# Performance work log

Hardware: AMD Instinct MI355X
Metric: run time of the kernel (lower is better)

Reference implementation:

```python
import jax, jax.numpy as jnp
import numpy as np

HEADS = 4
DIM_HEAD = 32
SCALE = 10.0
EPS = 1e-12  # F.normalize eps


def setup_inputs() -> dict:
    key = jax.random.key(0)
    k0, k1, k2 = jax.random.split(key, 3)
    b, c, h, w = 4, 256, 64, 64
    hidden = HEADS * DIM_HEAD  # 128
    x = jax.random.normal(k0, (b, c, h, w), dtype=jnp.float32)
    # 1x1 convs == per-pixel linear layers; store as [out_ch, in_ch]
    w_qkv = jax.random.normal(k1, (3 * hidden, c), dtype=jnp.float32) * (1.0 / np.sqrt(c))
    w_out = jax.random.normal(k2, (c, hidden), dtype=jnp.float32) * (1.0 / np.sqrt(hidden))
    b_out = jnp.zeros((c,), dtype=jnp.float32)
    return {"x": x, "w_qkv": w_qkv, "w_out": w_out, "b_out": b_out}


def _l2norm(t):
    # normalize along the per-head feature dim d (axis=2 of [b,h,d,n])
    n = jnp.sqrt(jnp.sum(t * t, axis=2, keepdims=True))
    return t / jnp.maximum(n, EPS)


def reference(x, w_qkv, w_out, b_out):
    b, c, h, w = x.shape
    n = h * w
    # to_qkv 1x1 conv (no bias)
    qkv = jnp.einsum('oc,bchw->bohw', w_qkv, x)          # [b, 3*hidden, h, w]
    qkv = qkv.reshape(b, 3, HEADS, DIM_HEAD, n)          # chunk dim=1 then split heads
    q, k, v = qkv[:, 0], qkv[:, 1], qkv[:, 2]            # each [b, heads, d, n]
    q = _l2norm(q)
    k = _l2norm(k)
    sim = jnp.einsum('bhdi,bhdj->bhij', q, k) * SCALE    # [b, heads, n, n]
    attn = jax.nn.softmax(sim, axis=-1)
    out = jnp.einsum('bhij,bhdj->bhid', attn, v)         # [b, heads, n, d]
    # 'b h (x y) d -> b (h d) x y'
    out = out.transpose(0, 1, 3, 2).reshape(b, HEADS * DIM_HEAD, h, w)
    # to_out 1x1 conv with bias
    return jnp.einsum('oc,bchw->bohw', w_out, out) + b_out[None, :, None, None]
```

## Files before the change

### kernel.cpp

```cpp
#include <hip/hip_runtime.h>
#include <math.h>

#define BB 4
#define CC 256
#define NHEAD 4
#define DH 32
#define NN 4096
#define HID 128

typedef _Float16 f16;
typedef _Float16 f16x8 __attribute__((ext_vector_type(8)));
typedef _Float16 f16x4 __attribute__((ext_vector_type(4)));
typedef float f32x4 __attribute__((ext_vector_type(4)));

#define QPRESCALE 14.42695041f
#define NSHIFT 14.42695041f

#if __has_builtin(__builtin_amdgcn_exp2f)
#define EXP2F(x) __builtin_amdgcn_exp2f(x)
#else
#define EXP2F(x) __expf((x)*0.6931471805599453f)
#endif

__device__ __forceinline__ f16x8 cvt8(const float* p) {
    float4 a = *(const float4*)p;
    float4 b = *(const float4*)(p + 4);
    f16x8 r;
    r[0] = (f16)a.x; r[1] = (f16)a.y; r[2] = (f16)a.z; r[3] = (f16)a.w;
    r[4] = (f16)b.x; r[5] = (f16)b.y; r[6] = (f16)b.z; r[7] = (f16)b.w;
    return r;
}

__global__ __launch_bounds__(256) void qkv_fused(const float* __restrict__ x,
                                                 const float* __restrict__ wq,
                                                 f16* __restrict__ qh,
                                                 f16* __restrict__ kh,
                                                 f16* __restrict__ vh) {
    int wave = threadIdx.x >> 6, lane = threadIdx.x & 63;
    int quad = lane >> 4, col = lane & 15;
    int b = blockIdx.z;
    int o0 = blockIdx.y * 64;
    int i0 = blockIdx.x * 128 + wave * 32;
    const float* xb = x + (size_t)b * CC * NN;

    f32x4 c[4][2];
#pragma unroll
    for (int mt = 0; mt < 4; mt++)
#pragma unroll
        for (int nt = 0; nt < 2; nt++) c[mt][nt] = f32x4{0.f, 0.f, 0.f, 0.f};

#pragma unroll
    for (int k0 = 0; k0 < CC; k0 += 32) {
        f16x8 a[4];
#pragma unroll
        for (int mt = 0; mt < 4; mt++)
            a[mt] = cvt8(wq + (size_t)(o0 + mt * 16 + col) * CC + k0 + quad * 8);
#pragma unroll
        for (int nt = 0; nt < 2; nt++) {
            const float* xc = xb + (size_t)(k0 + quad * 8) * NN + i0 + nt * 16 + col;
            f16x8 bf;
#pragma unroll
            for (int j = 0; j < 8; j++) bf[j] = (f16)xc[(size_t)j * NN];
#pragma unroll
            for (int mt = 0; mt < 4; mt++)
                c[mt][nt] = __builtin_amdgcn_mfma_f32_16x16x32_f16(a[mt], bf, c[mt][nt], 0, 0, 0);
        }
    }

    if (o0 < 256) {
        int isQ = (o0 < 128);
        int obase = isQ ? o0 : (o0 - 128);
        f16* dst = isQ ? qh : kh;
        float pre = isQ ? QPRESCALE : 1.0f;
#pragma unroll
        for (int nt = 0; nt < 2; nt++) {
#pragma unroll
            for (int hh = 0; hh < 2; hh++) {
                float ss = 0.f;
#pragma unroll
                for (int m2 = 0; m2 < 2; m2++)
#pragma unroll
                    for (int r = 0; r < 4; r++) {
                        float v = c[hh * 2 + m2][nt][r];
                        ss = fmaf(v, v, ss);
                    }
                ss += __shfl_xor(ss, 16);
                ss += __shfl_xor(ss, 32);
                float inv = pre / fmaxf(sqrtf(ss), 1e-12f);
                int h = (obase + hh * 32) >> 5;
                size_t row = ((size_t)(b * 4 + h) * NN + i0 + nt * 16 + col) * 32;
#pragma unroll
                for (int m2 = 0; m2 < 2; m2++) {
                    f16x4 st;
#pragma unroll
                    for (int r = 0; r < 4; r++) st[r] = (f16)(c[hh * 2 + m2][nt][r] * inv);
                    *(f16x4*)(dst + row + m2 * 16 + quad * 4) = st;
                }
            }
        }
    } else {
        int o2 = o0 - 256;
#pragma unroll
        for (int nt = 0; nt < 2; nt++) {
            int i = i0 + nt * 16 + col;
#pragma unroll
            for (int mt = 0; mt < 4; mt++) {
                int h = (o2 + mt * 16) >> 5;
                int d = (mt & 1) * 16 + quad * 4;
#pragma unroll
                for (int r = 0; r < 4; r++)
                    vh[((size_t)(b * 4 + h) * 32 + d + r) * NN + i] = (f16)c[mt][nt][r];
            }
        }
    }
}

#define KROW 40
#define VROW 72

struct KV32 {
    f16x8 k0, k1;
    f16x4 v0n0, v0n1, v1n0, v1n1;
};

__device__ __forceinline__ KV32 lds_frags(const f16* kl, const f16* vl,
                                          int jb, int col, int quad) {
    KV32 f;
    f.k0 = *(const f16x8*)(kl + (jb + col) * KROW + quad * 8);
    f.k1 = *(const f16x8*)(kl + (jb + 16 + col) * KROW + quad * 8);
    f.v0n0 = *(const f16x4*)(vl + col * VROW + jb + quad * 4);
    f.v0n1 = *(const f16x4*)(vl + (16 + col) * VROW + jb + quad * 4);
    f.v1n0 = *(const f16x4*)(vl + col * VROW + jb + 16 + quad * 4);
    f.v1n1 = *(const f16x4*)(vl + (16 + col) * VROW + jb + 16 + quad * 4);
    return f;
}

__device__ __forceinline__ f16x4 expblk(f32x4 s, float& lacc) {
    float p0 = EXP2F(s[0]), p1 = EXP2F(s[1]);
    float p2 = EXP2F(s[2]), p3 = EXP2F(s[3]);
    lacc += (p0 + p1) + (p2 + p3);
    f16x4 r;
    r[0] = (f16)p0; r[1] = (f16)p1; r[2] = (f16)p2; r[3] = (f16)p3;
    return r;
}

__device__ __forceinline__ void compute32(const KV32& f, f16x8 qB0, f16x8 qB1,
                                          f32x4& o00, f32x4& o01,
                                          f32x4& o10, f32x4& o11,
                                          float& l0, float& l1) {
    const f32x4 zs = {-NSHIFT, -NSHIFT, -NSHIFT, -NSHIFT};
    f32x4 s00 = __builtin_amdgcn_mfma_f32_16x16x32_f16(f.k0, qB0, zs, 0, 0, 0);
    f32x4 s10 = __builtin_amdgcn_mfma_f32_16x16x32_f16(f.k0, qB1, zs, 0, 0, 0);
    f32x4 s01 = __builtin_amdgcn_mfma_f32_16x16x32_f16(f.k1, qB0, zs, 0, 0, 0);
    f32x4 s11 = __builtin_amdgcn_mfma_f32_16x16x32_f16(f.k1, qB1, zs, 0, 0, 0);
    f16x4 p00 = expblk(s00, l0);
    f16x4 p10 = expblk(s10, l1);
    f16x4 p01 = expblk(s01, l0);
    f16x4 p11 = expblk(s11, l1);
    o00 = __builtin_amdgcn_mfma_f32_16x16x16f16(p00, f.v0n0, o00, 0, 0, 0);
    o01 = __builtin_amdgcn_mfma_f32_16x16x16f16(p00, f.v0n1, o01, 0, 0, 0);
    o10 = __builtin_amdgcn_mfma_f32_16x16x16f16(p10, f.v0n0, o10, 0, 0, 0);
    o11 = __builtin_amdgcn_mfma_f32_16x16x16f16(p10, f.v0n1, o11, 0, 0, 0);
    o00 = __builtin_amdgcn_mfma_f32_16x16x16f16(p01, f.v1n0, o00, 0, 0, 0);
    o01 = __builtin_amdgcn_mfma_f32_16x16x16f16(p01, f.v1n1, o01, 0, 0, 0);
    o10 = __builtin_amdgcn_mfma_f32_16x16x16f16(p11, f.v1n0, o10, 0, 0, 0);
    o11 = __builtin_amdgcn_mfma_f32_16x16x16f16(p11, f.v1n1, o11, 0, 0, 0);
}

template <int SPLIT>
__global__ __launch_bounds__(256, 4) void attn_mfma(const f16* __restrict__ qh,
                                                    const f16* __restrict__ kh,
                                                    const f16* __restrict__ vh,
                                                    float* __restrict__ op,
                                                    float* __restrict__ lp,
                                                    f16* __restrict__ att16) {
    __shared__ __align__(16) f16 klds[2][64 * KROW];
    __shared__ __align__(16) f16 vlds[2][32 * VROW];
    int t = threadIdx.x;
    int wave = t >> 6, lane = t & 63;
    int quad = lane >> 4, col = lane & 15;

    int bid = blockIdx.x;
    int xcd = bid & 7;
    int slot = bid >> 3;
    int bh = xcd * 2 + slot / (32 * SPLIT);
    int rem = slot % (32 * SPLIT);
    int s = rem >> 5;
    int i0 = (rem & 31) * 128;
    int iw = i0 + wave * 32;

    const int NT = 64 / SPLIT;
    int kbase = s * (NN / SPLIT);

    const f16* qb = qh + (size_t)bh * NN * 32;
    const f16* kb = kh + (size_t)bh * NN * 32 + (size_t)kbase * 32;
    const f16* vb = vh + (size_t)bh * 32 * NN + kbase;

    f16x8 qB0 = *(const f16x8*)(qb + (size_t)(iw + col) * 32 + quad * 8);
    f16x8 qB1 = *(const f16x8*)(qb + (size_t)(iw + 16 + col) * 32 + quad * 8);

    f32x4 o00 = {0.f, 0.f, 0.f, 0.f}, o01 = o00, o10 = o00, o11 = o00;
    float l0 = 0.f, l1 = 0.f;

    int ktr = t >> 2, kts = t & 3;
    int vtr = t >> 3, vts = t & 7;

    f16x8 kr, vr;
    kr = *(const f16x8*)(kb + (size_t)(0 + ktr) * 32 + kts * 8);
    vr = *(const f16x8*)(vb + (size_t)vtr * NN + 0 + vts * 8);
    *(f16x8*)(&klds[0][0] + ktr * KROW + kts * 8) = kr;
    *(f16x8*)(&vlds[0][0] + vtr * VROW + vts * 8) = vr;
    __syncthreads();
    kr = *(const f16x8*)(kb + (size_t)(64 + ktr) * 32 + kts * 8);
    vr = *(const f16x8*)(vb + (size_t)vtr * NN + 64 + vts * 8);

    for (int tile = 0; tile < NT - 2; tile++) {
        int buf = tile & 1;
        const f16* kl = &klds[buf][0];
        const f16* vl = &vlds[buf][0];
        KV32 f0 = lds_frags(kl, vl, 0, col, quad);
        KV32 f1 = lds_frags(kl, vl, 32, col, quad);
        compute32(f0, qB0, qB1, o00, o01, o10, o11, l0, l1);
        compute32(f1, qB0, qB1, o00, o01, o10, o11, l0, l1);
        *(f16x8*)(&klds[buf ^ 1][0] + ktr * KROW + kts * 8) = kr;
        *(f16x8*)(&vlds[buf ^ 1][0] + vtr * VROW + vts * 8) = vr;
        __syncthreads();
        int j0 = (tile + 2) * 64;
        kr = *(const f16x8*)(kb + (size_t)(j0 + ktr) * 32 + kts * 8);
        vr = *(const f16x8*)(vb + (size_t)vtr * NN + j0 + vts * 8);
    }
    {
        KV32 f0 = lds_frags(&klds[0][0], &vlds[0][0], 0, col, quad);
        KV32 f1 = lds_frags(&klds[0][0], &vlds[0][0], 32, col, quad);
        compute32(f0, qB0, qB1, o00, o01, o10, o11, l0, l1);
        compute32(f1, qB0, qB1, o00, o01, o10, o11, l0, l1);
        *(f16x8*)(&klds[1][0] + ktr * KROW + kts * 8) = kr;
        *(f16x8*)(&vlds[1][0] + vtr * VROW + vts * 8) = vr;
        __syncthreads();
    }
    {
        KV32 f0 = lds_frags(&klds[1][0], &vlds[1][0], 0, col, quad);
        KV32 f1 = lds_frags(&klds[1][0], &vlds[1][0], 32, col, quad);
        compute32(f0, qB0, qB1, o00, o01, o10, o11, l0, l1);
        compute32(f1, qB0, qB1, o00, o01, o10, o11, l0, l1);
    }

    l0 += __shfl_xor(l0, 16); l0 += __shfl_xor(l0, 32);
    l1 += __shfl_xor(l1, 16); l1 += __shfl_xor(l1, 32);

    if constexpr (SPLIT == 1) {
        int b = bh >> 2, h = bh & 3;
        f16* ab = att16 + (size_t)b * NN * HID + h * 32;
#pragma unroll
        for (int r = 0; r < 4; r++) {
            float inv0 = __builtin_amdgcn_rcpf(__shfl(l0, quad * 4 + r));
            float inv1 = __builtin_amdgcn_rcpf(__shfl(l1, quad * 4 + r));
            size_t row0 = (size_t)(iw + quad * 4 + r) * HID;
            size_t row1 = (size_t)(iw + 16 + quad * 4 + r) * HID;
            ab[row0 + col]      = (f16)(o00[r] * inv0);
            ab[row0 + 16 + col] = (f16)(o01[r] * inv0);
            ab[row1 + col]      = (f16)(o10[r] * inv1);
            ab[row1 + 16 + col] = (f16)(o11[r] * inv1);
        }
    } else {
        float* ob = op + (size_t)(s * 16 + bh) * NN * 32;
#pragma unroll
        for (int r = 0; r < 4; r++) {
            size_t r0 = (size_t)(iw + quad * 4 + r) * 32;
            size_t r1 = (size_t)(iw + 16 + quad * 4 + r) * 32;
            ob[r0 + col]      = o00[r];
            ob[r0 + 16 + col] = o01[r];
            ob[r1 + col]      = o10[r];
            ob[r1 + 16 + col] = o11[r];
        }
        if (quad == 0) {
            lp[(size_t)(s * 16 + bh) * NN + iw + col]      = l0;
            lp[(size_t)(s * 16 + bh) * NN + iw + 16 + col] = l1;
        }
    }
}

__global__ __launch_bounds__(256) void attn_combine(const float* __restrict__ op,
                                                    const float* __restrict__ lp,
                                                    f16* __restrict__ att16,
                                                    int nsplit) {
    int gid = blockIdx.x * 256 + threadIdx.x;
    int rowid = gid >> 3;
    int seg = gid & 7;
    int bh = rowid >> 12;
    int q = rowid & 4095;

    float l = 0.f;
    f32x4 acc = {0.f, 0.f, 0.f, 0.f};
    for (int s = 0; s < nsplit; s++) {
        l += lp[(size_t)(s * 16 + bh) * NN + q];
        f32x4 a = *(const f32x4*)(op + ((size_t)(s * 16 + bh) * NN + q) * 32 + seg * 4);
        acc += a;
    }
    float inv = __builtin_amdgcn_rcpf(l);
    int b = bh >> 2, h = bh & 3;
    f16x4 st;
    st[0] = (f16)(acc[0] * inv);
    st[1] = (f16)(acc[1] * inv);
    st[2] = (f16)(acc[2] * inv);
    st[3] = (f16)(acc[3] * inv);
    *(f16x4*)(att16 + ((size_t)b * NN + q) * HID + h * 32 + seg * 4) = st;
}

__global__ __launch_bounds__(256) void out_mfma(const f16* __restrict__ att16,
                                                const float* __restrict__ wo,
                                                const float* __restrict__ bo,
                                                float* __restrict__ out) {
    int wave = threadIdx.x >> 6, lane = threadIdx.x & 63;
    int quad = lane >> 4, col = lane & 15;
    int b = blockIdx.z;
    int i0 = (blockIdx.x * 4 + wave) * 32;
    int o0 = blockIdx.y * 64;
    const f16* ab = att16 + (size_t)b * NN * HID;

    const f32x4 z = {0.f, 0.f, 0.f, 0.f};
    f32x4 c[2][4];
#pragma unroll
    for (int it = 0; it < 2; it++)
#pragma unroll
        for (int ot = 0; ot < 4; ot++) c[it][ot] = z;

#pragma unroll
    for (int k0 = 0; k0 < HID; k0 += 32) {
        f16x8 a0 = *(const f16x8*)(ab + (size_t)(i0 + col) * HID + k0 + quad * 8);
        f16x8 a1 = *(const f16x8*)(ab + (size_t)(i0 + 16 + col) * HID + k0 + quad * 8);
#pragma unroll
        for (int ot = 0; ot < 4; ot++) {
            f16x8 bf = cvt8(wo + (size_t)(o0 + ot * 16 + col) * HID + k0 + quad * 8);
            c[0][ot] = __builtin_amdgcn_mfma_f32_16x16x32_f16(a0, bf, c[0][ot], 0, 0, 0);
            c[1][ot] = __builtin_amdgcn_mfma_f32_16x16x32_f16(a1, bf, c[1][ot], 0, 0, 0);
        }
    }

#pragma unroll
    for (int it = 0; it < 2; it++)
#pragma unroll
        for (int ot = 0; ot < 4; ot++) {
            int o = o0 + ot * 16 + col;
            float bias = bo[o];
            int i = i0 + it * 16 + quad * 4;
            float4 st = {c[it][ot][0] + bias, c[it][ot][1] + bias,
                         c[it][ot][2] + bias, c[it][ot][3] + bias};
            *(float4*)(out + ((size_t)b * CC + o) * NN + i) = st;
        }
}

extern "C" void kernel_launch(void* const* d_in, const int* in_sizes, int n_in,
                              void* d_out, int out_size, void* d_ws, size_t ws_size,
                              hipStream_t stream) {
    const float* x     = (const float*)d_in[0];
    const float* w_qkv = (const float*)d_in[1];
    const float* w_out = (const float*)d_in[2];
    const float* b_out = (const float*)d_in[3];
    float* out = (float*)d_out;

    char* ws = (char*)d_ws;
    f16* qh    = (f16*)(ws);
    f16* kh    = (f16*)(ws + (4u << 20));
    f16* vh    = (f16*)(ws + (8u << 20));
    f16* att16 = (f16*)(ws + (12u << 20));

    qkv_fused<<<dim3(NN / 128, 384 / 64, BB), 256, 0, stream>>>(x, w_qkv, qh, kh, vh);

    if (ws_size >= (50ull << 20)) {
        float* op = (float*)(ws + (16ull << 20));
        float* lp = (float*)(ws + (48ull << 20));
        attn_mfma<4><<<dim3(2048), 256, 0, stream>>>(qh, kh, vh, op, lp, att16);
        attn_combine<<<dim3(2048), 256, 0, stream>>>(op, lp, att16, 4);
    } else if (ws_size >= (33ull << 20)) {
        float* op = (float*)(ws + (16ull << 20));
        float* lp = (float*)(ws + (32ull << 20));
        attn_mfma<2><<<dim3(1024), 256, 0, stream>>>(qh, kh, vh, op, lp, att16);
        attn_combine<<<dim3(2048), 256, 0, stream>>>(op, lp, att16, 2);
    } else {
        attn_mfma<1><<<dim3(512), 256, 0, stream>>>(qh, kh, vh, nullptr, nullptr, att16);
    }

    out_mfma<<<dim3(NN / 128, CC / 64, BB), 256, 0, stream>>>(att16, w_out, b_out, out);
}
```

Before: 165.3 us.

## Use K=32 MFMA for PV with permuted K rows and MFMA row-sum

```diff
diff --git a/kernel.cpp b/kernel.cpp
--- a/kernel.cpp
+++ b/kernel.cpp
@@ -11,7 +11,9 @@
 typedef _Float16 f16;
 typedef _Float16 f16x8 __attribute__((ext_vector_type(8)));
 typedef _Float16 f16x4 __attribute__((ext_vector_type(4)));
+typedef _Float16 f16x2 __attribute__((ext_vector_type(2)));
 typedef float f32x4 __attribute__((ext_vector_type(4)));
+typedef unsigned int u32x4 __attribute__((ext_vector_type(4)));
 
 #define QPRESCALE 14.42695041f
 #define NSHIFT 14.42695041f
@@ -118,53 +120,53 @@
 #define KROW 40
 #define VROW 72
 
-struct KV32 {
-    f16x8 k0, k1;
-    f16x4 v0n0, v0n1, v1n0, v1n1;
+struct G32 {
+    f16x8 kA, kB;
+    f16x8 v0, v1;
 };
 
-__device__ __forceinline__ KV32 lds_frags(const f16* kl, const f16* vl,
-                                          int jb, int col, int quad) {
-    KV32 f;
-    f.k0 = *(const f16x8*)(kl + (jb + col) * KROW + quad * 8);
-    f.k1 = *(const f16x8*)(kl + (jb + 16 + col) * KROW + quad * 8);
-    f.v0n0 = *(const f16x4*)(vl + col * VROW + jb + quad * 4);
-    f.v0n1 = *(const f16x4*)(vl + (16 + col) * VROW + jb + quad * 4);
-    f.v1n0 = *(const f16x4*)(vl + col * VROW + jb + 16 + quad * 4);
-    f.v1n1 = *(const f16x4*)(vl + (16 + col) * VROW + jb + 16 + quad * 4);
+__device__ __forceinline__ G32 lds_frags32(const f16* kl, const f16* vl,
+                                           int jb, int col, int quad) {
+    G32 f;
+    f.kA = *(const f16x8*)(kl + (jb + col) * KROW + quad * 8);
+    f.kB = *(const f16x8*)(kl + (jb + 16 + col) * KROW + quad * 8);
+    f.v0 = *(const f16x8*)(vl + col * VROW + jb + quad * 8);
+    f.v1 = *(const f16x8*)(vl + (16 + col) * VROW + jb + quad * 8);
     return f;
 }
 
-__device__ __forceinline__ f16x4 expblk(f32x4 s, float& lacc) {
-    float p0 = EXP2F(s[0]), p1 = EXP2F(s[1]);
-    float p2 = EXP2F(s[2]), p3 = EXP2F(s[3]);
-    lacc += (p0 + p1) + (p2 + p3);
-    f16x4 r;
-    r[0] = (f16)p0; r[1] = (f16)p1; r[2] = (f16)p2; r[3] = (f16)p3;
-    return r;
-}
-
-__device__ __forceinline__ void compute32(const KV32& f, f16x8 qB0, f16x8 qB1,
-                                          f32x4& o00, f32x4& o01,
-                                          f32x4& o10, f32x4& o11,
-                                          float& l0, float& l1) {
+__device__ __forceinline__ f16x8 expblk2(f32x4 sa, f32x4 sb) {
+    u32x4 w;
+    w[0] = __builtin_bit_cast(unsigned int,
+            __builtin_amdgcn_cvt_pkrtz(EXP2F(sa[0]), EXP2F(sa[1])));
+    w[1] = __builtin_bit_cast(unsigned int,
+            __builtin_amdgcn_cvt_pkrtz(EXP2F(sa[2]), EXP2F(sa[3])));
+    w[2] = __builtin_bit_cast(unsigned int,
+            __builtin_amdgcn_cvt_pkrtz(EXP2F(sb[0]), EXP2F(sb[1])));
+    w[3] = __builtin_bit_cast(unsigned int,
+            __builtin_amdgcn_cvt_pkrtz(EXP2F(sb[2]), EXP2F(sb[3])));
+    return __builtin_bit_cast(f16x8, w);
+}
+
+__device__ __forceinline__ void compute32g(const G32& f, f16x8 qB0, f16x8 qB1,
+                                           f32x4& o00, f32x4& o01,
+                                           f32x4& o10, f32x4& o11,
+                                           f32x4& lf0, f32x4& lf1) {
     const f32x4 zs = {-NSHIFT, -NSHIFT, -NSHIFT, -NSHIFT};
-    f32x4 s00 = __builtin_amdgcn_mfma_f32_16x16x32_f16(f.k0, qB0, zs, 0, 0, 0);
-    f32x4 s10 = __builtin_amdgcn_mfma_f32_16x16x32_f16(f.k0, qB1, zs, 0, 0, 0);
-    f32x4 s01 = __builtin_amdgcn_mfma_f32_16x16x32_f16(f.k1, qB0, zs, 0, 0, 0);
-    f32x4 s11 = __builtin_amdgcn_mfma_f32_16x16x32_f16(f.k1, qB1, zs, 0, 0, 0);
-    f16x4 p00 = expblk(s00, l0);
-    f16x4 p10 = expblk(s10, l1);
-    f16x4 p01 = expblk(s01, l0);
-    f16x4 p11 = expblk(s11, l1);
-    o00 = __builtin_amdgcn_mfma_f32_16x16x16f16(p00, f.v0n0, o00, 0, 0, 0);
-    o01 = __builtin_amdgcn_mfma_f32_16x16x16f16(p00, f.v0n1, o01, 0, 0, 0);
-    o10 = __builtin_amdgcn_mfma_f32_16x16x16f16(p10, f.v0n0, o10, 0, 0, 0);
-    o11 = __builtin_amdgcn_mfma_f32_16x16x16f16(p10, f.v0n1, o11, 0, 0, 0);
-    o00 = __builtin_amdgcn_mfma_f32_16x16x16f16(p01, f.v1n0, o00, 0, 0, 0);
-    o01 = __builtin_amdgcn_mfma_f32_16x16x16f16(p01, f.v1n1, o01, 0, 0, 0);
-    o10 = __builtin_amdgcn_mfma_f32_16x16x16f16(p11, f.v1n0, o10, 0, 0, 0);
-    o11 = __builtin_amdgcn_mfma_f32_16x16x16f16(p11, f.v1n1, o11, 0, 0, 0);
+    f16 one = (f16)1.0f;
+    f16x8 ones = {one, one, one, one, one, one, one, one};
+    f32x4 sa0 = __builtin_amdgcn_mfma_f32_16x16x32_f16(f.kA, qB0, zs, 0, 0, 0);
+    f32x4 sb0 = __builtin_amdgcn_mfma_f32_16x16x32_f16(f.kB, qB0, zs, 0, 0, 0);
+    f32x4 sa1 = __builtin_amdgcn_mfma_f32_16x16x32_f16(f.kA, qB1, zs, 0, 0, 0);
+    f32x4 sb1 = __builtin_amdgcn_mfma_f32_16x16x32_f16(f.kB, qB1, zs, 0, 0, 0);
+    f16x8 p0 = expblk2(sa0, sb0);
+    f16x8 p1 = expblk2(sa1, sb1);
+    o00 = __builtin_amdgcn_mfma_f32_16x16x32_f16(p0, f.v0, o00, 0, 0, 0);
+    o01 = __builtin_amdgcn_mfma_f32_16x16x32_f16(p0, f.v1, o01, 0, 0, 0);
+    lf0 = __builtin_amdgcn_mfma_f32_16x16x32_f16(p0, ones, lf0, 0, 0, 0);
+    o10 = __builtin_amdgcn_mfma_f32_16x16x32_f16(p1, f.v0, o10, 0, 0, 0);
+    o11 = __builtin_amdgcn_mfma_f32_16x16x32_f16(p1, f.v1, o11, 0, 0, 0);
+    lf1 = __builtin_amdgcn_mfma_f32_16x16x32_f16(p1, ones, lf1, 0, 0, 0);
 }
 
 template <int SPLIT>
@@ -200,61 +202,59 @@
     f16x8 qB1 = *(const f16x8*)(qb + (size_t)(iw + 16 + col) * 32 + quad * 8);
 
     f32x4 o00 = {0.f, 0.f, 0.f, 0.f}, o01 = o00, o10 = o00, o11 = o00;
-    float l0 = 0.f, l1 = 0.f;
+    f32x4 lf0 = o00, lf1 = o00;
 
     int ktr = t >> 2, kts = t & 3;
+    int ksrc = (ktr & 32) | ((ktr & 12) << 1) | ((ktr & 16) >> 2) | (ktr & 3);
     int vtr = t >> 3, vts = t & 7;
 
     f16x8 kr, vr;
-    kr = *(const f16x8*)(kb + (size_t)(0 + ktr) * 32 + kts * 8);
+    kr = *(const f16x8*)(kb + (size_t)(0 + ksrc) * 32 + kts * 8);
     vr = *(const f16x8*)(vb + (size_t)vtr * NN + 0 + vts * 8);
     *(f16x8*)(&klds[0][0] + ktr * KROW + kts * 8) = kr;
     *(f16x8*)(&vlds[0][0] + vtr * VROW + vts * 8) = vr;
     __syncthreads();
-    kr = *(const f16x8*)(kb + (size_t)(64 + ktr) * 32 + kts * 8);
+    kr = *(const f16x8*)(kb + (size_t)(64 + ksrc) * 32 + kts * 8);
     vr = *(const f16x8*)(vb + (size_t)vtr * NN + 64 + vts * 8);
 
     for (int tile = 0; tile < NT - 2; tile++) {
         int buf = tile & 1;
         const f16* kl = &klds[buf][0];
         const f16* vl = &vlds[buf][0];
-        KV32 f0 = lds_frags(kl, vl, 0, col, quad);
-        KV32 f1 = lds_frags(kl, vl, 32, col, quad);
-        compute32(f0, qB0, qB1, o00, o01, o10, o11, l0, l1);
-        compute32(f1, qB0, qB1, o00, o01, o10, o11, l0, l1);
+        G32 g0 = lds_frags32(kl, vl, 0, col, quad);
+        G32 g1 = lds_frags32(kl, vl, 32, col, quad);
+        compute32g(g0, qB0, qB1, o00, o01, o10, o11, lf0, lf1);
+        compute32g(g1, qB0, qB1, o00, o01, o10, o11, lf0, lf1);
         *(f16x8*)(&klds[buf ^ 1][0] + ktr * KROW + kts * 8) = kr;
         *(f16x8*)(&vlds[buf ^ 1][0] + vtr * VROW + vts * 8) = vr;
         __syncthreads();
         int j0 = (tile + 2) * 64;
-        kr = *(const f16x8*)(kb + (size_t)(j0 + ktr) * 32 + kts * 8);
+        kr = *(const f16x8*)(kb + (size_t)(j0 + ksrc) * 32 + kts * 8);
         vr = *(const f16x8*)(vb + (size_t)vtr * NN + j0 + vts * 8);
     }
     {
-        KV32 f0 = lds_frags(&klds[0][0], &vlds[0][0], 0, col, quad);
-        KV32 f1 = lds_frags(&klds[0][0], &vlds[0][0], 32, col, quad);
-        compute32(f0, qB0, qB1, o00, o01, o10, o11, l0, l1);
-        compute32(f1, qB0, qB1, o00, o01, o10, o11, l0, l1);
+        G32 g0 = lds_frags32(&klds[0][0], &vlds[0][0], 0, col, quad);
+        G32 g1 = lds_frags32(&klds[0][0], &vlds[0][0], 32, col, quad);
+        compute32g(g0, qB0, qB1, o00, o01, o10, o11, lf0, lf1);
+        compute32g(g1, qB0, qB1, o00, o01, o10, o11, lf0, lf1);
         *(f16x8*)(&klds[1][0] + ktr * KROW + kts * 8) = kr;
         *(f16x8*)(&vlds[1][0] + vtr * VROW + vts * 8) = vr;
         __syncthreads();
     }
     {
-        KV32 f0 = lds_frags(&klds[1][0], &vlds[1][0], 0, col, quad);
-        KV32 f1 = lds_frags(&klds[1][0], &vlds[1][0], 32, col, quad);
-        compute32(f0, qB0, qB1, o00, o01, o10, o11, l0, l1);
-        compute32(f1, qB0, qB1, o00, o01, o10, o11, l0, l1);
-    }
-
-    l0 += __shfl_xor(l0, 16); l0 += __shfl_xor(l0, 32);
-    l1 += __shfl_xor(l1, 16); l1 += __shfl_xor(l1, 32);
+        G32 g0 = lds_frags32(&klds[1][0], &vlds[1][0], 0, col, quad);
+        G32 g1 = lds_frags32(&klds[1][0], &vlds[1][0], 32, col, quad);
+        compute32g(g0, qB0, qB1, o00, o01, o10, o11, lf0, lf1);
+        compute32g(g1, qB0, qB1, o00, o01, o10, o11, lf0, lf1);
+    }
 
     if constexpr (SPLIT == 1) {
         int b = bh >> 2, h = bh & 3;
         f16* ab = att16 + (size_t)b * NN * HID + h * 32;
 #pragma unroll
         for (int r = 0; r < 4; r++) {
-            float inv0 = __builtin_amdgcn_rcpf(__shfl(l0, quad * 4 + r));
-            float inv1 = __builtin_amdgcn_rcpf(__shfl(l1, quad * 4 + r));
+            float inv0 = __builtin_amdgcn_rcpf(lf0[r]);
+            float inv1 = __builtin_amdgcn_rcpf(lf1[r]);
             size_t row0 = (size_t)(iw + quad * 4 + r) * HID;
             size_t row1 = (size_t)(iw + 16 + quad * 4 + r) * HID;
             ab[row0 + col]      = (f16)(o00[r] * inv0);
@@ -273,9 +273,13 @@
             ob[r1 + col]      = o10[r];
             ob[r1 + 16 + col] = o11[r];
         }
-        if (quad == 0) {
-            lp[(size_t)(s * 16 + bh) * NN + iw + col]      = l0;
-            lp[(size_t)(s * 16 + bh) * NN + iw + 16 + col] = l1;
+        if (col == 0) {
+            float* lb = lp + (size_t)(s * 16 + bh) * NN;
+#pragma unroll
+            for (int r = 0; r < 4; r++) {
+                lb[iw + quad * 4 + r]      = lf0[r];
+                lb[iw + 16 + quad * 4 + r] = lf1[r];
+            }
         }
     }
 }
```

Result: faster. 158.6 us (-4.1%).
